# Performance work log

Measured on AMD Instinct MI355X. Metric: run time of the kernel, lower is better.

## Reference

```python
import jax, jax.numpy as jnp
import numpy as np

B, L, E = 2, 2048, 1024
NH, DH = 16, 64          # num_heads, attn_hidden_size
HID = 4096               # FFN hidden_size
EPS = 1e-5


def _layernorm(x, g, b):
    mu = jnp.mean(x, axis=-1, keepdims=True)
    var = jnp.var(x, axis=-1, keepdims=True)
    return (x - mu) * jax.lax.rsqrt(var + EPS) * g + b


def setup_inputs() -> dict:
    key = jax.random.key(0)
    ks = jax.random.split(key, 12)
    s = 0.02
    return {
        "x":    jax.random.normal(ks[0], (B, L, E), dtype=jnp.float32),
        "Wa":   jax.random.normal(ks[1], (E, NH * 3 * DH), dtype=jnp.float32) * s,
        "Wout": jax.random.normal(ks[2], (NH * DH, E), dtype=jnp.float32) * s,
        "bout": jnp.zeros((E,), dtype=jnp.float32),
        "W1":   jax.random.normal(ks[3], (E, HID), dtype=jnp.float32) * s,
        "b1":   jnp.zeros((HID,), dtype=jnp.float32),
        "W2":   jax.random.normal(ks[4], (HID, E), dtype=jnp.float32) * s,
        "b2":   jnp.zeros((E,), dtype=jnp.float32),
        "g1":   jnp.ones((E,), dtype=jnp.float32),
        "be1":  jnp.zeros((E,), dtype=jnp.float32),
        "g2":   jnp.ones((E,), dtype=jnp.float32),
        "be2":  jnp.zeros((E,), dtype=jnp.float32),
    }


def _attention(o, Wa, Wout, bout):
    b, l, e = o.shape
    tmp = o @ Wa                                   # (b, l, nh*3*dh)
    tmp = tmp.reshape(b, l, NH, 3 * DH).transpose(0, 2, 1, 3)  # (b, nh, l, 3dh)
    q, k, v = jnp.split(tmp, 3, axis=-1)           # each (b, nh, l, dh)
    scores = jnp.einsum('bhqd,bhkd->bhqk', q, k) / np.sqrt(DH)
    causal = jnp.tril(jnp.ones((l, l), dtype=bool))
    scores = jnp.where(causal, scores, -jnp.inf)
    A = jax.nn.softmax(scores, axis=-1)
    out = jnp.einsum('bhqk,bhkd->bhqd', A, v)      # (b, nh, l, dh)
    out = out.transpose(0, 2, 1, 3).reshape(b, l, NH * DH)
    return out @ Wout + bout


def reference(x, Wa, Wout, bout, W1, b1, W2, b2, g1, be1, g2, be2):
    o = _layernorm(x, g1, be1)
    o = _attention(o, Wa, Wout, bout)
    o = _layernorm(x + o, g2, be2)
    o = o @ W1 + b1          # activation is Identity
    o = x + (o @ W2 + b2)
    return o
```

## Files before the change

### kernel.cpp

```cpp
#include <hip/hip_runtime.h>
#include <hip/hip_bf16.h>

#define BB 2
#define LL 2048
#define EE 1024
#define NHH 16
#define DHH 64
#define HIDD 4096
#define MTOK (BB*LL)
#define NQKV (NHH*3*DHH)

typedef __attribute__((ext_vector_type(8))) short bf16x8;
typedef __attribute__((ext_vector_type(4))) float f32x4;

#define MFMA16(a,b,c) __builtin_amdgcn_mfma_f32_16x16x32_bf16(a,b,c,0,0,0)

static __device__ __forceinline__ void gload_lds16(const void* g, void* lds) {
  __builtin_amdgcn_global_load_lds(
      (const __attribute__((address_space(1))) unsigned int*)g,
      (__attribute__((address_space(3))) unsigned int*)lds, 16, 0, 0);
}

__global__ __launch_bounds__(256)
void convT_kernel(const float* __restrict__ W, __hip_bfloat16* __restrict__ WT,
                  int K, int N) {
  __shared__ float tile[32][33];
  const int tx = threadIdx.x & 31, ty = threadIdx.x >> 5;
  const int n0 = blockIdx.x * 32, k0 = blockIdx.y * 32;
#pragma unroll
  for (int i = 0; i < 4; ++i)
    tile[ty + i*8][tx] = W[(size_t)(k0 + ty + i*8) * N + n0 + tx];
  __syncthreads();
#pragma unroll
  for (int i = 0; i < 4; ++i)
    WT[(size_t)(n0 + ty + i*8) * K + k0 + tx] = __float2bfloat16(tile[tx][ty + i*8]);
}

__global__ __launch_bounds__(256)
void vtrans_kernel(const __hip_bfloat16* __restrict__ qkv,
                   __hip_bfloat16* __restrict__ VT) {
  __shared__ ushort tile[32][34];
  const int tx = threadIdx.x & 31, ty = threadIdx.x >> 5;
  const int tok0 = blockIdx.x * 32;
  const int dh0  = blockIdx.y * 32;
  const int bh   = blockIdx.z;
  const int b = bh >> 4, h = bh & 15;
  const ushort* src = (const ushort*)qkv;
#pragma unroll
  for (int i = 0; i < 4; ++i)
    tile[ty + i*8][tx] =
      src[(size_t)(b*LL + tok0 + ty + i*8) * NQKV + h*192 + 128 + dh0 + tx];
  __syncthreads();
  ushort* dst = (ushort*)VT;
#pragma unroll
  for (int i = 0; i < 4; ++i)
    dst[(size_t)(bh*DHH + dh0 + ty + i*8) * LL + tok0 + tx] = tile[tx][ty + i*8];
}

__global__ __launch_bounds__(256)
void ln_kernel(const float* __restrict__ in, const float* __restrict__ g,
               const float* __restrict__ be, __hip_bfloat16* __restrict__ out) {
  const int row = blockIdx.x;
  const int t = threadIdx.x;
  const float4 v = ((const float4*)(in + (size_t)row * EE))[t];
  float s = v.x + v.y + v.z + v.w;
  float q = v.x*v.x + v.y*v.y + v.z*v.z + v.w*v.w;
#pragma unroll
  for (int off = 32; off >= 1; off >>= 1) {
    s += __shfl_xor(s, off);
    q += __shfl_xor(q, off);
  }
  __shared__ float ps[4], pq[4];
  if ((t & 63) == 0) { ps[t >> 6] = s; pq[t >> 6] = q; }
  __syncthreads();
  s = ps[0] + ps[1] + ps[2] + ps[3];
  q = pq[0] + pq[1] + pq[2] + pq[3];
  const float mean = s * (1.0f / EE);
  const float rstd = rsqrtf(q * (1.0f / EE) - mean * mean + 1e-5f);
  const float4 gg = ((const float4*)g)[t];
  const float4 bb = ((const float4*)be)[t];
  union { ushort4 u; __hip_bfloat16 h[4]; } o;
  o.h[0] = __float2bfloat16((v.x - mean) * rstd * gg.x + bb.x);
  o.h[1] = __float2bfloat16((v.y - mean) * rstd * gg.y + bb.y);
  o.h[2] = __float2bfloat16((v.z - mean) * rstd * gg.z + bb.z);
  o.h[3] = __float2bfloat16((v.w - mean) * rstd * gg.w + bb.w);
  ((ushort4*)(out + (size_t)row * EE))[t] = o.u;
}

template<int BN, int OUT_BF16, int HAS_BIAS, int HAS_RES>
__device__ __forceinline__ void gemm_body(
    const __hip_bfloat16* __restrict__ A, const __hip_bfloat16* __restrict__ BT,
    void* __restrict__ Cv, const float* __restrict__ bias,
    const float* __restrict__ res, int M, int N, int K, int lda, int ldb) {
  constexpr int NF = BN / 32;
  __shared__ alignas(16) __hip_bfloat16 sA[2][128 * 32];
  __shared__ alignas(16) __hip_bfloat16 sB[2][BN * 32];
  const int t = threadIdx.x;
  const int wv = t >> 6, l = t & 63;
  const int lr = l & 15, lk = (l >> 4) * 8;

  const int nwg = gridDim.x * gridDim.y;
  int wg = blockIdx.y * gridDim.x + blockIdx.x;
  wg = (wg & 7) * (nwg >> 3) + (wg >> 3);
  const int bx = wg % gridDim.x, by = wg / gridDim.x;
  const int m0 = by * 128, n0 = bx * BN;

  const int wrow = (wv >> 1) * 64;
  const int wcol = (wv & 1) * (BN / 2);
  const int srow = t >> 2, scol = (t & 3) * 8;
  const __hip_bfloat16* gA = A + (size_t)(m0 + srow) * lda + scol;
  const __hip_bfloat16* gB = BT + (size_t)(n0 + srow) * ldb + scol;

  auto stage = [&](int buf, int k0) {
    char* dA = (char*)(&sA[buf][0]) + wv * 1024;
    gload_lds16(gA + k0, dA);
    gload_lds16(gA + (size_t)64 * lda + k0, dA + 4096);
    char* dB = (char*)(&sB[buf][0]) + wv * 1024;
    gload_lds16(gB + k0, dB);
    if constexpr (BN == 128)
      gload_lds16(gB + (size_t)64 * ldb + k0, dB + 4096);
  };

  f32x4 acc[4][NF] = {};

  auto compute = [&](int buf) {
    bf16x8 af[4], bfv[NF];
#pragma unroll
    for (int mi = 0; mi < 4; ++mi)
      af[mi] = *(const bf16x8*)(&sA[buf][(wrow + mi * 16 + lr) * 32 + lk]);
#pragma unroll
    for (int ni = 0; ni < NF; ++ni)
      bfv[ni] = *(const bf16x8*)(&sB[buf][(wcol + ni * 16 + lr) * 32 + lk]);
#pragma unroll
    for (int mi = 0; mi < 4; ++mi)
#pragma unroll
      for (int ni = 0; ni < NF; ++ni)
        acc[mi][ni] = MFMA16(af[mi], bfv[ni], acc[mi][ni]);
  };

  stage(0, 0);
  __syncthreads();
  for (int k0 = 0; k0 < K; k0 += 64) {
    stage(1, k0 + 32);
    compute(0);
    __syncthreads();
    if (k0 + 64 < K) stage(0, k0 + 64);
    compute(1);
    __syncthreads();
  }

  const int rbase = (l >> 4) * 4;
#pragma unroll
  for (int mi = 0; mi < 4; ++mi) {
#pragma unroll
    for (int ni = 0; ni < NF; ++ni) {
#pragma unroll
      for (int r = 0; r < 4; ++r) {
        const int row = m0 + wrow + mi * 16 + rbase + r;
        const int col = n0 + wcol + ni * 16 + lr;
        float v = acc[mi][ni][r];
        if constexpr (HAS_BIAS) v += bias[col];
        if constexpr (HAS_RES)  v += res[(size_t)row * N + col];
        if constexpr (OUT_BF16)
          ((__hip_bfloat16*)Cv)[(size_t)row * N + col] = __float2bfloat16(v);
        else
          ((float*)Cv)[(size_t)row * N + col] = v;
      }
    }
  }
}

__global__ __launch_bounds__(256)
void gemm_qkv(const __hip_bfloat16* A, const __hip_bfloat16* BT, __hip_bfloat16* C) {
  gemm_body<128,1,0,0>(A, BT, C, nullptr, nullptr, MTOK, NQKV, EE, EE, EE);
}
__global__ __launch_bounds__(256)
void gemm_wout(const __hip_bfloat16* A, const __hip_bfloat16* BT, float* C,
               const float* bias, const float* res) {
  gemm_body<128,0,1,1>(A, BT, C, bias, res, MTOK, EE, EE, EE, EE);
}
__global__ __launch_bounds__(256)
void gemm_ffn1(const __hip_bfloat16* A, const __hip_bfloat16* BT, __hip_bfloat16* C,
               const float* bias) {
  gemm_body<128,1,1,0>(A, BT, C, bias, nullptr, MTOK, HIDD, EE, EE, EE);
}
__global__ __launch_bounds__(256)
void gemm_ffn2p(const __hip_bfloat16* A, const __hip_bfloat16* BT,
                float* P0, float* P1) {
  const int ks = blockIdx.z;
  float* P = ks ? P1 : P0;
  gemm_body<64,0,0,0>(A + ks * 2048, BT + ks * 2048, P, nullptr, nullptr,
                      MTOK, EE, 2048, HIDD, HIDD);
}

__global__ __launch_bounds__(256)
void ffn2_reduce(const float4* __restrict__ P0, const float4* __restrict__ P1,
                 const float4* __restrict__ x, const float* __restrict__ b2,
                 float4* __restrict__ out) {
  const int n4 = MTOK * EE / 4;
  for (int i = blockIdx.x * 256 + threadIdx.x; i < n4; i += 2048 * 256) {
    const float4 b = ((const float4*)b2)[i & 255];
    const float4 p = P0[i], q = P1[i], xx = x[i];
    float4 o;
    o.x = xx.x + b.x + p.x + q.x;
    o.y = xx.y + b.y + p.y + q.y;
    o.z = xx.z + b.z + p.z + q.z;
    o.w = xx.w + b.w + p.w + q.w;
    out[i] = o;
  }
}

__global__ __launch_bounds__(256)
void attn_kernel(const __hip_bfloat16* __restrict__ qkv,
                 const __hip_bfloat16* __restrict__ VT,
                 __hip_bfloat16* __restrict__ out) {
  __shared__ alignas(16) __hip_bfloat16 sP[4][32 * 72];
  const int t = threadIdx.x;
  const int wv = t >> 6, l = t & 63;
  const int lr = l & 15, lg = l >> 4, lk = lg * 8;
  const int hh = blockIdx.y, b = blockIdx.z;
  int qx = blockIdx.x;
  if (b == 1) qx = 15 - qx;
  const int qw = qx * 128 + wv * 32;
  const size_t rowbase = (size_t)b * LL;
  const int hoff = hh * (3 * DHH);
  const __hip_bfloat16* vt = VT + (size_t)((b * NHH + hh) * DHH) * LL;

  bf16x8 qa[2][2];
#pragma unroll
  for (int rg = 0; rg < 2; ++rg)
#pragma unroll
    for (int h = 0; h < 2; ++h)
      qa[rg][h] = *(const bf16x8*)(qkv + (rowbase + qw + rg*16 + lr) * NQKV
                                   + hoff + h*32 + lk);

  f32x4 o[2][4] = {};
  float mrun[2][4], lrun[2][4];
#pragma unroll
  for (int rg = 0; rg < 2; ++rg)
#pragma unroll
    for (int r = 0; r < 4; ++r) { mrun[rg][r] = -INFINITY; lrun[rg][r] = 0.f; }

  __hip_bfloat16* sp = sP[wv];
  const int nt = (qw + 95) >> 6;

  for (int kt = 0; kt < nt; ++kt) {
    const int t0 = kt * 64;
    bf16x8 vb[4][2];
#pragma unroll
    for (int ni = 0; ni < 4; ++ni)
#pragma unroll
      for (int ks = 0; ks < 2; ++ks)
        vb[ni][ks] = *(const bf16x8*)(vt + (size_t)(ni*16 + lr) * LL + t0 + ks*32 + lk);

    f32x4 s[2][4];
#pragma unroll
    for (int tg = 0; tg < 4; ++tg) {
      const __hip_bfloat16* kp = qkv + (rowbase + t0 + tg*16 + lr) * NQKV + hoff + DHH;
      bf16x8 kb0 = *(const bf16x8*)(kp + lk);
      bf16x8 kb1 = *(const bf16x8*)(kp + 32 + lk);
#pragma unroll
      for (int rg = 0; rg < 2; ++rg) {
        f32x4 z = {0.f, 0.f, 0.f, 0.f};
        z = MFMA16(qa[rg][0], kb0, z);
        z = MFMA16(qa[rg][1], kb1, z);
        s[rg][tg] = z;
      }
    }

    const bool edge = (kt == nt - 1);
#pragma unroll
    for (int rg = 0; rg < 2; ++rg)
#pragma unroll
      for (int tg = 0; tg < 4; ++tg)
#pragma unroll
        for (int r = 0; r < 4; ++r) {
          float v = s[rg][tg][r] * 0.125f;
          if (edge) {
            const int tok = t0 + tg*16 + lr;
            const int qr  = qw + rg*16 + lg*4 + r;
            if (tok > qr) v = -INFINITY;
          }
          s[rg][tg][r] = v;
        }

#pragma unroll
    for (int rg = 0; rg < 2; ++rg)
#pragma unroll
      for (int r = 0; r < 4; ++r) {
        float m = fmaxf(fmaxf(s[rg][0][r], s[rg][1][r]),
                        fmaxf(s[rg][2][r], s[rg][3][r]));
#pragma unroll
        for (int off = 8; off >= 1; off >>= 1)
          m = fmaxf(m, __shfl_xor(m, off));
        const float mnew = fmaxf(mrun[rg][r], m);
        const float corr = __expf(mrun[rg][r] - mnew);
        const float p0 = __expf(s[rg][0][r] - mnew);
        const float p1 = __expf(s[rg][1][r] - mnew);
        const float p2 = __expf(s[rg][2][r] - mnew);
        const float p3 = __expf(s[rg][3][r] - mnew);
        float rs = (p0 + p1) + (p2 + p3);
#pragma unroll
        for (int off = 8; off >= 1; off >>= 1)
          rs += __shfl_xor(rs, off);
        lrun[rg][r] = lrun[rg][r] * corr + rs;
        mrun[rg][r] = mnew;
        const int q = rg*16 + lg*4 + r;
        sp[q*72 +      lr] = __float2bfloat16(p0);
        sp[q*72 + 16 + lr] = __float2bfloat16(p1);
        sp[q*72 + 32 + lr] = __float2bfloat16(p2);
        sp[q*72 + 48 + lr] = __float2bfloat16(p3);
#pragma unroll
        for (int ni = 0; ni < 4; ++ni) o[rg][ni][r] *= corr;
      }

#pragma unroll
    for (int rg = 0; rg < 2; ++rg) {
      bf16x8 pf0 = *(const bf16x8*)(sp + (rg*16 + lr)*72 + lk);
      bf16x8 pf1 = *(const bf16x8*)(sp + (rg*16 + lr)*72 + 32 + lk);
#pragma unroll
      for (int ni = 0; ni < 4; ++ni) {
        o[rg][ni] = MFMA16(pf0, vb[ni][0], o[rg][ni]);
        o[rg][ni] = MFMA16(pf1, vb[ni][1], o[rg][ni]);
      }
    }
  }

#pragma unroll
  for (int rg = 0; rg < 2; ++rg)
#pragma unroll
    for (int r = 0; r < 4; ++r) {
      const float inv = 1.0f / lrun[rg][r];
      const int qr = qw + rg*16 + lg*4 + r;
      __hip_bfloat16* op = out + (rowbase + qr) * (NHH * DHH) + hh * DHH;
#pragma unroll
      for (int ni = 0; ni < 4; ++ni)
        op[ni*16 + lr] = __float2bfloat16(o[rg][ni][r] * inv);
    }
}

extern "C" void kernel_launch(void* const* d_in, const int* in_sizes, int n_in,
                              void* d_out, int out_size, void* d_ws, size_t ws_size,
                              hipStream_t stream) {
  (void)in_sizes; (void)n_in; (void)out_size; (void)ws_size;
  const float* x    = (const float*)d_in[0];
  const float* Wa   = (const float*)d_in[1];
  const float* Wout = (const float*)d_in[2];
  const float* bout = (const float*)d_in[3];
  const float* W1   = (const float*)d_in[4];
  const float* b1   = (const float*)d_in[5];
  const float* W2   = (const float*)d_in[6];
  const float* b2   = (const float*)d_in[7];
  const float* g1   = (const float*)d_in[8];
  const float* be1  = (const float*)d_in[9];
  const float* g2   = (const float*)d_in[10];
  const float* be2  = (const float*)d_in[11];

  char* ws = (char*)d_ws;
  __hip_bfloat16* WaT   = (__hip_bfloat16*)(ws + 0);
  __hip_bfloat16* WoutT = (__hip_bfloat16*)(ws + 6291456);
  __hip_bfloat16* W1T   = (__hip_bfloat16*)(ws + 8388608);
  __hip_bfloat16* W2T   = (__hip_bfloat16*)(ws + 16777216);
  __hip_bfloat16* o1    = (__hip_bfloat16*)(ws + 25165824);
  __hip_bfloat16* qkv   = (__hip_bfloat16*)(ws + 33554432);
  __hip_bfloat16* VT    = (__hip_bfloat16*)(ws + 58720256);
  __hip_bfloat16* attnb = (__hip_bfloat16*)(ws + 67108864);
  float*          ybuf  = (float*)(ws + 33554432);
  __hip_bfloat16* ln2b  = (__hip_bfloat16*)(ws + 25165824);
  __hip_bfloat16* hbuf  = (__hip_bfloat16*)(ws + 50331648);
  float*          P0    = (float*)(ws + 0);
  float*          P1    = (float*)(ws + 33554432);

  convT_kernel<<<dim3(NQKV/32, EE/32), 256, 0, stream>>>(Wa, WaT, EE, NQKV);
  convT_kernel<<<dim3(EE/32, EE/32), 256, 0, stream>>>(Wout, WoutT, EE, EE);
  convT_kernel<<<dim3(HIDD/32, EE/32), 256, 0, stream>>>(W1, W1T, EE, HIDD);
  convT_kernel<<<dim3(EE/32, HIDD/32), 256, 0, stream>>>(W2, W2T, HIDD, EE);
  ln_kernel<<<MTOK, 256, 0, stream>>>(x, g1, be1, o1);
  gemm_qkv<<<dim3(NQKV/128, MTOK/128), 256, 0, stream>>>(o1, WaT, qkv);
  vtrans_kernel<<<dim3(LL/32, DHH/32, BB*NHH), 256, 0, stream>>>(qkv, VT);
  attn_kernel<<<dim3(LL/128, NHH, BB), 256, 0, stream>>>(qkv, VT, attnb);
  gemm_wout<<<dim3(EE/128, MTOK/128), 256, 0, stream>>>(attnb, WoutT, ybuf, bout, x);
  ln_kernel<<<MTOK, 256, 0, stream>>>(ybuf, g2, be2, ln2b);
  gemm_ffn1<<<dim3(HIDD/128, MTOK/128), 256, 0, stream>>>(ln2b, W1T, hbuf, b1);
  gemm_ffn2p<<<dim3(EE/64, MTOK/128, 2), 256, 0, stream>>>(hbuf, W2T, P0, P1);
  ffn2_reduce<<<2048, 256, 0, stream>>>((const float4*)P0, (const float4*)P1,
                                        (const float4*)x, b2, (float4*)d_out);
}
```

Measured before the change: 402.4 us.

## Shrink attention waves to 16 query rows with transposed S for lane-local softmax

The attention kernel now gives each wave 16 query rows instead of 32 and launches twice as many blocks, which raises parallelism and improves causal load balance. It computes S transposed (K as the A operand) so each lane holds scores for a single query. This reduces the row max and sum reductions to two cross-group shuffles, and P is written to LDS with packed 8-byte stores. It also adds s_setprio around the MFMA sections. In exchange, each K/V fragment load now feeds only one query group, which doubles K/V global traffic per query, and a shuffle is needed to redistribute the correction factors.

New measurement: 442.9 us. +10.1%, slower.

```diff
diff --git a/kernel.cpp b/kernel.cpp
--- a/kernel.cpp
+++ b/kernel.cpp
@@ -214,35 +214,30 @@
 void attn_kernel(const __hip_bfloat16* __restrict__ qkv,
                  const __hip_bfloat16* __restrict__ VT,
                  __hip_bfloat16* __restrict__ out) {
-  __shared__ alignas(16) __hip_bfloat16 sP[4][32 * 72];
+  __shared__ alignas(16) __hip_bfloat16 sP[4][16 * 72];
   const int t = threadIdx.x;
   const int wv = t >> 6, l = t & 63;
   const int lr = l & 15, lg = l >> 4, lk = lg * 8;
   const int hh = blockIdx.y, b = blockIdx.z;
   int qx = blockIdx.x;
-  if (b == 1) qx = 15 - qx;
-  const int qw = qx * 128 + wv * 32;
+  if (b == 1) qx = 31 - qx;
+  const int qw = qx * 64 + wv * 16;
   const size_t rowbase = (size_t)b * LL;
   const int hoff = hh * (3 * DHH);
   const __hip_bfloat16* vt = VT + (size_t)((b * NHH + hh) * DHH) * LL;
 
-  bf16x8 qa[2][2];
-#pragma unroll
-  for (int rg = 0; rg < 2; ++rg)
-#pragma unroll
-    for (int h = 0; h < 2; ++h)
-      qa[rg][h] = *(const bf16x8*)(qkv + (rowbase + qw + rg*16 + lr) * NQKV
-                                   + hoff + h*32 + lk);
-
-  f32x4 o[2][4] = {};
-  float mrun[2][4], lrun[2][4];
-#pragma unroll
-  for (int rg = 0; rg < 2; ++rg)
-#pragma unroll
-    for (int r = 0; r < 4; ++r) { mrun[rg][r] = -INFINITY; lrun[rg][r] = 0.f; }
-
+  bf16x8 qa0, qa1;
+  {
+    const __hip_bfloat16* qp = qkv + (rowbase + qw + lr) * NQKV + hoff;
+    qa0 = *(const bf16x8*)(qp + lk);
+    qa1 = *(const bf16x8*)(qp + 32 + lk);
+  }
+
+  f32x4 o[4] = {};
+  float mrun = -INFINITY, lrun = 0.f;
   __hip_bfloat16* sp = sP[wv];
-  const int nt = (qw + 95) >> 6;
+  const __hip_bfloat16* kbase = qkv + rowbase * NQKV + hoff + DHH;
+  const int nt = (qw + 79) >> 6;
 
   for (int kt = 0; kt < nt; ++kt) {
     const int t0 = kt * 64;
@@ -253,90 +248,87 @@
       for (int ks = 0; ks < 2; ++ks)
         vb[ni][ks] = *(const bf16x8*)(vt + (size_t)(ni*16 + lr) * LL + t0 + ks*32 + lk);
 
-    f32x4 s[2][4];
+    f32x4 st[4];
+    __builtin_amdgcn_s_setprio(1);
 #pragma unroll
     for (int tg = 0; tg < 4; ++tg) {
-      const __hip_bfloat16* kp = qkv + (rowbase + t0 + tg*16 + lr) * NQKV + hoff + DHH;
+      const __hip_bfloat16* kp = kbase + (size_t)(t0 + tg*16 + lr) * NQKV;
       bf16x8 kb0 = *(const bf16x8*)(kp + lk);
       bf16x8 kb1 = *(const bf16x8*)(kp + 32 + lk);
-#pragma unroll
-      for (int rg = 0; rg < 2; ++rg) {
-        f32x4 z = {0.f, 0.f, 0.f, 0.f};
-        z = MFMA16(qa[rg][0], kb0, z);
-        z = MFMA16(qa[rg][1], kb1, z);
-        s[rg][tg] = z;
+      f32x4 z = {0.f, 0.f, 0.f, 0.f};
+      z = MFMA16(kb0, qa0, z);
+      z = MFMA16(kb1, qa1, z);
+      st[tg] = z;
+    }
+    __builtin_amdgcn_s_setprio(0);
+
+    const bool edge = (kt == nt - 1);
+    float tmax = -INFINITY;
+#pragma unroll
+    for (int tg = 0; tg < 4; ++tg)
+#pragma unroll
+      for (int r = 0; r < 4; ++r) {
+        float v = st[tg][r] * 0.125f;
+        if (edge && (t0 + tg*16 + lg*4 + r > qw + lr)) v = -INFINITY;
+        st[tg][r] = v;
+        tmax = fmaxf(tmax, v);
       }
+    tmax = fmaxf(tmax, __shfl_xor(tmax, 16));
+    tmax = fmaxf(tmax, __shfl_xor(tmax, 32));
+    const float mnew = fmaxf(mrun, tmax);
+    const float corr = __expf(mrun - mnew);
+    float rs = 0.f;
+#pragma unroll
+    for (int tg = 0; tg < 4; ++tg) {
+      const float p0 = __expf(st[tg][0] - mnew);
+      const float p1 = __expf(st[tg][1] - mnew);
+      const float p2 = __expf(st[tg][2] - mnew);
+      const float p3 = __expf(st[tg][3] - mnew);
+      rs += (p0 + p1) + (p2 + p3);
+      union { ushort4 u; __hip_bfloat16 h[4]; } pk;
+      pk.h[0] = __float2bfloat16(p0);
+      pk.h[1] = __float2bfloat16(p1);
+      pk.h[2] = __float2bfloat16(p2);
+      pk.h[3] = __float2bfloat16(p3);
+      *(ushort4*)(sp + lr*72 + tg*16 + lg*4) = pk.u;
     }
-
-    const bool edge = (kt == nt - 1);
-#pragma unroll
-    for (int rg = 0; rg < 2; ++rg)
-#pragma unroll
-      for (int tg = 0; tg < 4; ++tg)
-#pragma unroll
-        for (int r = 0; r < 4; ++r) {
-          float v = s[rg][tg][r] * 0.125f;
-          if (edge) {
-            const int tok = t0 + tg*16 + lr;
-            const int qr  = qw + rg*16 + lg*4 + r;
-            if (tok > qr) v = -INFINITY;
-          }
-          s[rg][tg][r] = v;
-        }
-
-#pragma unroll
-    for (int rg = 0; rg < 2; ++rg)
-#pragma unroll
-      for (int r = 0; r < 4; ++r) {
-        float m = fmaxf(fmaxf(s[rg][0][r], s[rg][1][r]),
-                        fmaxf(s[rg][2][r], s[rg][3][r]));
-#pragma unroll
-        for (int off = 8; off >= 1; off >>= 1)
-          m = fmaxf(m, __shfl_xor(m, off));
-        const float mnew = fmaxf(mrun[rg][r], m);
-        const float corr = __expf(mrun[rg][r] - mnew);
-        const float p0 = __expf(s[rg][0][r] - mnew);
-        const float p1 = __expf(s[rg][1][r] - mnew);
-        const float p2 = __expf(s[rg][2][r] - mnew);
-        const float p3 = __expf(s[rg][3][r] - mnew);
-        float rs = (p0 + p1) + (p2 + p3);
-#pragma unroll
-        for (int off = 8; off >= 1; off >>= 1)
-          rs += __shfl_xor(rs, off);
-        lrun[rg][r] = lrun[rg][r] * corr + rs;
-        mrun[rg][r] = mnew;
-        const int q = rg*16 + lg*4 + r;
-        sp[q*72 +      lr] = __float2bfloat16(p0);
-        sp[q*72 + 16 + lr] = __float2bfloat16(p1);
-        sp[q*72 + 32 + lr] = __float2bfloat16(p2);
-        sp[q*72 + 48 + lr] = __float2bfloat16(p3);
-#pragma unroll
-        for (int ni = 0; ni < 4; ++ni) o[rg][ni][r] *= corr;
-      }
-
-#pragma unroll
-    for (int rg = 0; rg < 2; ++rg) {
-      bf16x8 pf0 = *(const bf16x8*)(sp + (rg*16 + lr)*72 + lk);
-      bf16x8 pf1 = *(const bf16x8*)(sp + (rg*16 + lr)*72 + 32 + lk);
-#pragma unroll
-      for (int ni = 0; ni < 4; ++ni) {
-        o[rg][ni] = MFMA16(pf0, vb[ni][0], o[rg][ni]);
-        o[rg][ni] = MFMA16(pf1, vb[ni][1], o[rg][ni]);
-      }
+    rs += __shfl_xor(rs, 16);
+    rs += __shfl_xor(rs, 32);
+    lrun = lrun * corr + rs;
+    mrun = mnew;
+
+    float corr_o[4];
+#pragma unroll
+    for (int r = 0; r < 4; ++r)
+      corr_o[r] = __shfl(corr, lg*20 + r);
+#pragma unroll
+    for (int ni = 0; ni < 4; ++ni)
+#pragma unroll
+      for (int r = 0; r < 4; ++r) o[ni][r] *= corr_o[r];
+
+    bf16x8 pf0 = *(const bf16x8*)(sp + lr*72 + lk);
+    bf16x8 pf1 = *(const bf16x8*)(sp + lr*72 + 32 + lk);
+    __builtin_amdgcn_s_setprio(1);
+#pragma unroll
+    for (int ni = 0; ni < 4; ++ni) {
+      o[ni] = MFMA16(pf0, vb[ni][0], o[ni]);
+      o[ni] = MFMA16(pf1, vb[ni][1], o[ni]);
     }
-  }
-
-#pragma unroll
-  for (int rg = 0; rg < 2; ++rg)
-#pragma unroll
-    for (int r = 0; r < 4; ++r) {
-      const float inv = 1.0f / lrun[rg][r];
-      const int qr = qw + rg*16 + lg*4 + r;
-      __hip_bfloat16* op = out + (rowbase + qr) * (NHH * DHH) + hh * DHH;
-#pragma unroll
-      for (int ni = 0; ni < 4; ++ni)
-        op[ni*16 + lr] = __float2bfloat16(o[rg][ni][r] * inv);
-    }
+    __builtin_amdgcn_s_setprio(0);
+  }
+
+  float linv[4];
+#pragma unroll
+  for (int r = 0; r < 4; ++r)
+    linv[r] = 1.0f / __shfl(lrun, lg*20 + r);
+#pragma unroll
+  for (int r = 0; r < 4; ++r) {
+    const int qr = qw + lg*4 + r;
+    __hip_bfloat16* op = out + (rowbase + qr) * (NHH * DHH) + hh * DHH;
+#pragma unroll
+    for (int ni = 0; ni < 4; ++ni)
+      op[ni*16 + lr] = __float2bfloat16(o[ni][r] * linv[r]);
+  }
 }
 
 extern "C" void kernel_launch(void* const* d_in, const int* in_sizes, int n_in,
@@ -378,7 +370,7 @@
   ln_kernel<<<MTOK, 256, 0, stream>>>(x, g1, be1, o1);
   gemm_qkv<<<dim3(NQKV/128, MTOK/128), 256, 0, stream>>>(o1, WaT, qkv);
   vtrans_kernel<<<dim3(LL/32, DHH/32, BB*NHH), 256, 0, stream>>>(qkv, VT);
-  attn_kernel<<<dim3(LL/128, NHH, BB), 256, 0, stream>>>(qkv, VT, attnb);
+  attn_kernel<<<dim3(LL/64, NHH, BB), 256, 0, stream>>>(qkv, VT, attnb);
   gemm_wout<<<dim3(EE/128, MTOK/128), 256, 0, stream>>>(attnb, WoutT, ybuf, bout, x);
   ln_kernel<<<MTOK, 256, 0, stream>>>(ybuf, g2, be2, ln2b);
   gemm_ffn1<<<dim3(HIDD/128, MTOK/128), 256, 0, stream>>>(ln2b, W1T, hbuf, b1);
```
